# Kernel tuning notes

Hardware: AMD Instinct MI355X
Metric: run time of the kernel (lower is better)

Reference implementation:

```python
import jax, jax.numpy as jnp
import numpy as np

GRID_SIZE = 5
SPLINE_ORDER = 3
IN_FEAT = 320   # 32 * 10
OUT_FEAT = 2048 # 32 * 64
BN_EPS = 1e-3


def make_grid():
    # efficient-kan grid buffer: (in_features, grid_size + 2*spline_order + 1)
    h = 2.0 / GRID_SIZE  # grid_range = [-1, 1]
    g = jnp.arange(-SPLINE_ORDER, GRID_SIZE + SPLINE_ORDER + 1, dtype=jnp.float32) * h - 1.0
    return jnp.broadcast_to(g, (IN_FEAT, g.shape[0]))  # (320, 12)


def b_splines(x, grid):
    # x: (B, In) -> bases: (B, In, grid_size + spline_order)
    x = x[..., None]  # (B, In, 1)
    bases = ((x >= grid[:, :-1]) & (x < grid[:, 1:])).astype(x.dtype)
    for k in range(1, SPLINE_ORDER + 1):
        left = (x - grid[:, : -(k + 1)]) / (grid[:, k:-1] - grid[:, : -(k + 1)])
        right = (grid[:, k + 1:] - x) / (grid[:, k + 1:] - grid[:, 1:-k])
        bases = left * bases[..., :-1] + right * bases[..., 1:]
    return bases


def setup_inputs() -> dict:
    key = jax.random.key(0)
    ks = jax.random.split(key, 8)
    N = 40000
    inputs = jax.random.normal(ks[0], (N, 32, 10), dtype=jnp.float32)
    linear_w = jax.random.normal(ks[1], (64, 10), dtype=jnp.float32) * 0.1
    base_weight = jax.random.normal(ks[2], (OUT_FEAT, IN_FEAT), dtype=jnp.float32) * 0.02
    spline_weight = jax.random.normal(ks[3], (OUT_FEAT, IN_FEAT, GRID_SIZE + SPLINE_ORDER), dtype=jnp.float32) * 0.02
    spline_scaler = jax.random.normal(ks[4], (OUT_FEAT, IN_FEAT), dtype=jnp.float32) * 0.1 + 1.0
    bn_gamma = jax.random.normal(ks[5], (64,), dtype=jnp.float32) * 0.1 + 1.0
    bn_beta = jax.random.normal(ks[6], (64,), dtype=jnp.float32) * 0.1
    bn_mean = jnp.zeros((64,), dtype=jnp.float32)
    bn_var = jax.random.uniform(ks[7], (64,), dtype=jnp.float32, minval=0.5, maxval=1.5)
    return {
        "inputs": inputs,
        "linear_w": linear_w,
        "base_weight": base_weight,
        "spline_weight": spline_weight,
        "spline_scaler": spline_scaler,
        "bn_gamma": bn_gamma,
        "bn_beta": bn_beta,
        "bn_mean": bn_mean,
        "bn_var": bn_var,
    }


def reference(inputs, linear_w, base_weight, spline_weight, spline_scaler,
              bn_gamma, bn_beta, bn_mean, bn_var):
    N = inputs.shape[0]
    # plain linear path: (N, 32, 10) -> (N, 32, 64). (The torch chunking over
    # self.part is mathematically identical to one matmul.)
    x_linear = jnp.einsum('npi,oi->npo', inputs, linear_w)
    # KAN path on flattened pillars: (N, 320)
    xk = inputs.reshape(N, IN_FEAT)
    grid = make_grid()
    base_out = jnp.matmul(jax.nn.silu(xk), base_weight.T)  # (N, 2048)
    bases = b_splines(xk, grid)  # (N, 320, 8)
    scaled_spline_w = (spline_weight * spline_scaler[..., None]).reshape(OUT_FEAT, -1)
    spline_out = jnp.matmul(bases.reshape(N, -1), scaled_spline_w.T)  # (N, 2048)
    x_kan = (base_out + spline_out).reshape(N, 32, 64)
    x = x_linear + x_kan
    # BatchNorm1d over the channel (last) dim, inference mode, eps=1e-3
    inv_std = jax.lax.rsqrt(bn_var + BN_EPS)
    x = (x - bn_mean) * (inv_std * bn_gamma) + bn_beta
    x = jax.nn.relu(x)
    x_max = jnp.max(x, axis=1, keepdims=True)  # (N, 1, 64)
    x_rep = jnp.broadcast_to(x_max, x.shape)   # repeat over 32 points
    return jnp.concatenate([x, x_rep], axis=2)  # (N, 32, 128)
```

## Files before the change

kernel.cpp:

```cpp
#include <hip/hip_runtime.h>
#include <cstdint>
#include <math.h>

#define IN_FEAT 320
#define OUT_FEAT 2048
#define NB 8
#define KSIL 320
#define KTOT 2880
#define BM 128
#define BN 128
#define BK 32
#define LDA 40
#define BN_EPS 1e-3f
#define A_OFF ((size_t)16 << 20)

typedef __bf16 bf16;
typedef __attribute__((ext_vector_type(8))) __bf16 bf16x8;
typedef __attribute__((ext_vector_type(4))) float f32x4;

__device__ __forceinline__ void bspline8(float xv, float* b) {
    float xc = (xv + 2.2f) * 2.5f;
    float cf = floorf(xc);
    int c = (int)cf;
    float t = xc - cf;
    float omt = 1.0f - t;
    float t2 = t * t, t3 = t2 * t;
    float w0 = omt * omt * omt * (1.0f / 6.0f);
    float w1 = (3.0f * t3 - 6.0f * t2 + 4.0f) * (1.0f / 6.0f);
    float w2 = (-3.0f * t3 + 3.0f * t2 + 3.0f * t + 1.0f) * (1.0f / 6.0f);
    float w3 = t3 * (1.0f / 6.0f);
    if (xc < 0.0f) { w0 = w1 = w2 = w3 = 0.0f; }
#pragma unroll
    for (int j = 0; j < 8; ++j) {
        int d = c - j;
        b[j] = (d == 3) ? w0 : (d == 2) ? w1 : (d == 1) ? w2 : (d == 0) ? w3 : 0.0f;
    }
}

__device__ __forceinline__ bf16x8 pack8(const float* f) {
    bf16x8 v;
#pragma unroll
    for (int j = 0; j < 8; ++j) v[j] = (bf16)f[j];
    return v;
}

__device__ __forceinline__ void gl2lds16(const bf16* g, bf16* l) {
    __builtin_amdgcn_global_load_lds(
        (const __attribute__((address_space(1))) void*)g,
        (__attribute__((address_space(3))) void*)l, 16, 0, 0);
}

__global__ __launch_bounds__(256) void prep_w(const float* __restrict__ bw,
                                              const float* __restrict__ sw,
                                              const float* __restrict__ ss,
                                              bf16* __restrict__ W) {
    const int k = blockIdx.x * 256 + threadIdx.x;
    const int o = blockIdx.y;
    if (k >= KTOT) return;
    float w;
    if (k < KSIL) {
        w = bw[o * IN_FEAT + k];
    } else {
        const int s = k - KSIL;
        const int i = s >> 3, j = s & 7;
        w = sw[(o * IN_FEAT + i) * NB + j] * ss[o * IN_FEAT + i];
    }
    W[o * KTOT + k] = (bf16)w;
}

__global__ __launch_bounds__(256) void prep_a(const float* __restrict__ x,
                                              bf16* __restrict__ A, int total) {
    const int t = blockIdx.x * 256 + threadIdx.x;
    if (t >= total) return;
    const int row = t / IN_FEAT;
    const int f = t - row * IN_FEAT;
    const float xv = x[t];
    A[(size_t)row * KTOT + f] = (bf16)(xv / (1.0f + __expf(-xv)));
    float b[8];
    bspline8(xv, b);
    *(bf16x8*)&A[(size_t)row * KTOT + KSIL + f * 8] = pack8(b);
}

__global__ __launch_bounds__(256)
void pfn_gemm_ws(const float* __restrict__ x, const bf16* __restrict__ A,
                 const bf16* __restrict__ W, const float* __restrict__ lw,
                 const float* __restrict__ gamma, const float* __restrict__ beta,
                 const float* __restrict__ mean, const float* __restrict__ var,
                 float* __restrict__ out, int N, int nbx) {
    __shared__ bf16 As[BM * BK];
    __shared__ bf16 Bs[BN * BK];

    const int blk = blockIdx.x;
    const int sid = blk >> 9;
    const int t = blk & 511;
    const int by = t >> 5;
    const int bx = (sid << 5) + (t & 31);
    if (bx >= nbx) return;

    const int row0 = bx * BM;
    const int col0 = by * BN;
    const int tid = threadIdx.x;
    const int wave = tid >> 6;
    const int lane = tid & 63;
    const int wr = wave >> 1;
    const int wc = wave & 1;
    const int l15 = lane & 15;
    const int quad = lane >> 4;

    const int r0 = tid >> 2;
    const int s0 = tid & 3;
    const int g0 = s0 ^ ((r0 >> 1) & 3);
    const bf16* a0 = A + (size_t)(row0 + r0) * KTOT + g0 * 8;
    const bf16* a1 = a0 + (size_t)64 * KTOT;
    const bf16* b0 = W + (size_t)(col0 + r0) * KTOT + g0 * 8;
    const bf16* b1 = b0 + (size_t)64 * KTOT;
    bf16* lA0 = As + tid * 8;
    bf16* lA1 = As + (tid + 256) * 8;
    bf16* lB0 = Bs + tid * 8;
    bf16* lB1 = Bs + (tid + 256) * 8;

    const int sfr = quad ^ ((l15 >> 1) & 3);

    f32x4 acc[4][4] = {};

    for (int kc = 0; kc < KTOT; kc += BK) {
        __syncthreads();
        gl2lds16(a0 + kc, lA0);
        gl2lds16(a1 + kc, lA1);
        gl2lds16(b0 + kc, lB0);
        gl2lds16(b1 + kc, lB1);
        __syncthreads();
        bf16x8 af[4], bv[4];
#pragma unroll
        for (int i = 0; i < 4; ++i)
            af[i] = *(const bf16x8*)&As[(wr * 64 + i * 16 + l15) * BK + sfr * 8];
#pragma unroll
        for (int j = 0; j < 4; ++j)
            bv[j] = *(const bf16x8*)&Bs[(wc * 64 + j * 16 + l15) * BK + sfr * 8];
#pragma unroll
        for (int i = 0; i < 4; ++i)
#pragma unroll
            for (int j = 0; j < 4; ++j)
                acc[i][j] = __builtin_amdgcn_mfma_f32_16x16x32_bf16(af[i], bv[j],
                                                                   acc[i][j], 0, 0, 0);
    }

    const int p = by * 2 + wc;
    float sc[4], sh[4];
#pragma unroll
    for (int j = 0; j < 4; ++j) {
        const int c = j * 16 + l15;
        const float s = rsqrtf(var[c] + BN_EPS) * gamma[c];
        sc[j] = s;
        sh[j] = beta[c] - mean[c] * s;
    }
#pragma unroll
    for (int i = 0; i < 4; ++i) {
#pragma unroll
        for (int reg = 0; reg < 4; ++reg) {
            const int row = row0 + wr * 64 + i * 16 + quad * 4 + reg;
            if (row >= N) continue;
            float xq[10];
            const float* xp = &x[(size_t)row * IN_FEAT + p * 10];
#pragma unroll
            for (int q = 0; q < 10; ++q) xq[q] = xp[q];
#pragma unroll
            for (int j = 0; j < 4; ++j) {
                const int c = j * 16 + l15;
                float v = acc[i][j][reg];
#pragma unroll
                for (int q = 0; q < 10; ++q) v = fmaf(xq[q], lw[c * 10 + q], v);
                v = fmaxf(v * sc[j] + sh[j], 0.0f);
                out[((size_t)row * 32 + p) * 128 + c] = v;
            }
        }
    }
}

template <bool HASW>
__global__ __launch_bounds__(256)
void pfn_gemm(const float* __restrict__ x, const bf16* __restrict__ W,
              const float* __restrict__ bw, const float* __restrict__ sw,
              const float* __restrict__ ss, const float* __restrict__ lw,
              const float* __restrict__ gamma, const float* __restrict__ beta,
              const float* __restrict__ mean, const float* __restrict__ var,
              float* __restrict__ out, int N) {
    __shared__ bf16 As[BM * LDA];
    __shared__ bf16 Bs[BN * LDA];
    const int tid = threadIdx.x;
    const int row0 = blockIdx.x * BM;
    const int col0 = blockIdx.y * BN;
    const int wave = tid >> 6;
    const int lane = tid & 63;
    const int wr = wave >> 1;
    const int wc = wave & 1;
    const int l15 = lane & 15;
    const int quad = lane >> 4;
    f32x4 acc[4][4] = {};
    auto stage_b = [&](int kc) {
        const int ol = tid >> 1;
        const int k0 = (tid & 1) * 16;
        if (HASW) {
            const bf16x8* src = (const bf16x8*)&W[(size_t)(col0 + ol) * KTOT + kc + k0];
            *(bf16x8*)&Bs[ol * LDA + k0] = src[0];
            *(bf16x8*)&Bs[ol * LDA + k0 + 8] = src[1];
        } else {
            const int o = col0 + ol;
#pragma unroll
            for (int u = 0; u < 16; ++u) {
                const int gk = kc + k0 + u;
                float w;
                if (gk < KSIL) {
                    w = bw[o * IN_FEAT + gk];
                } else {
                    const int s = gk - KSIL;
                    const int i = s >> 3, j = s & 7;
                    w = sw[(o * IN_FEAT + i) * NB + j] * ss[o * IN_FEAT + i];
                }
                Bs[ol * LDA + k0 + u] = (bf16)w;
            }
        }
    };
    auto mma_step = [&]() {
        bf16x8 af[4], bv[4];
#pragma unroll
        for (int i = 0; i < 4; ++i)
            af[i] = *(const bf16x8*)&As[(wr * 64 + i * 16 + l15) * LDA + quad * 8];
#pragma unroll
        for (int j = 0; j < 4; ++j)
            bv[j] = *(const bf16x8*)&Bs[(wc * 64 + j * 16 + l15) * LDA + quad * 8];
#pragma unroll
        for (int i = 0; i < 4; ++i)
#pragma unroll
            for (int j = 0; j < 4; ++j)
                acc[i][j] = __builtin_amdgcn_mfma_f32_16x16x32_bf16(af[i], bv[j],
                                                                   acc[i][j], 0, 0, 0);
    };
    for (int kc = 0; kc < KSIL; kc += BK) {
        __syncthreads();
        stage_b(kc);
        {
            const int r = tid >> 1;
            const int k0 = (tid & 1) * 16;
            const int row = row0 + r;
            float v[16];
            if (row < N) {
                const float* xp = &x[(size_t)row * IN_FEAT + kc + k0];
#pragma unroll
                for (int u = 0; u < 16; ++u) {
                    const float xv = xp[u];
                    v[u] = xv / (1.0f + __expf(-xv));
                }
            } else {
#pragma unroll
                for (int u = 0; u < 16; ++u) v[u] = 0.0f;
            }
            *(bf16x8*)&As[r * LDA + k0] = pack8(v);
            *(bf16x8*)&As[r * LDA + k0 + 8] = pack8(v + 8);
        }
        __syncthreads();
        mma_step();
    }
    for (int kc = KSIL; kc < KTOT; kc += BK) {
        __syncthreads();
        stage_b(kc);
        {
            const int i0 = (kc - KSIL) >> 3;
#pragma unroll
            for (int s = 0; s < 2; ++s) {
                const int task = tid + s * 256;
                const int r = task >> 2;
                const int f = task & 3;
                const int row = row0 + r;
                float b[8];
                if (row < N) {
                    bspline8(x[(size_t)row * IN_FEAT + i0 + f], b);
                } else {
#pragma unroll
                    for (int j = 0; j < 8; ++j) b[j] = 0.0f;
                }
                *(bf16x8*)&As[r * LDA + f * 8] = pack8(b);
            }
        }
        __syncthreads();
        mma_step();
    }
    const int p = blockIdx.y * 2 + wc;
    float sc[4], sh[4];
#pragma unroll
    for (int j = 0; j < 4; ++j) {
        const int c = j * 16 + l15;
        const float s = rsqrtf(var[c] + BN_EPS) * gamma[c];
        sc[j] = s;
        sh[j] = beta[c] - mean[c] * s;
    }
#pragma unroll
    for (int i = 0; i < 4; ++i) {
#pragma unroll
        for (int reg = 0; reg < 4; ++reg) {
            const int row = row0 + wr * 64 + i * 16 + quad * 4 + reg;
            if (row >= N) continue;
            float xq[10];
            const float* xp = &x[(size_t)row * IN_FEAT + p * 10];
#pragma unroll
            for (int q = 0; q < 10; ++q) xq[q] = xp[q];
#pragma unroll
            for (int j = 0; j < 4; ++j) {
                const int c = j * 16 + l15;
                float v = acc[i][j][reg];
#pragma unroll
                for (int q = 0; q < 10; ++q) v = fmaf(xq[q], lw[c * 10 + q], v);
                v = fmaxf(v * sc[j] + sh[j], 0.0f);
                out[((size_t)row * 32 + p) * 128 + c] = v;
            }
        }
    }
}

__global__ __launch_bounds__(256) void pfn_maxcat(float* __restrict__ out, int N) {
    const int n = blockIdx.x;
    const int c = threadIdx.x & 63;
    const int g = threadIdx.x >> 6;
    __shared__ float red[4][64];
    float m = 0.0f;
    for (int pp = g; pp < 32; pp += 4)
        m = fmaxf(m, out[((size_t)n * 32 + pp) * 128 + c]);
    red[g][c] = m;
    __syncthreads();
    m = fmaxf(fmaxf(red[0][c], red[1][c]), fmaxf(red[2][c], red[3][c]));
    for (int pp = g; pp < 32; pp += 4)
        out[((size_t)n * 32 + pp) * 128 + 64 + c] = m;
}

extern "C" void kernel_launch(void* const* d_in, const int* in_sizes, int n_in,
                              void* d_out, int out_size, void* d_ws, size_t ws_size,
                              hipStream_t stream) {
    const float* x     = (const float*)d_in[0];
    const float* lw    = (const float*)d_in[1];
    const float* bw    = (const float*)d_in[2];
    const float* sw    = (const float*)d_in[3];
    const float* ss    = (const float*)d_in[4];
    const float* gamma = (const float*)d_in[5];
    const float* beta  = (const float*)d_in[6];
    const float* mean  = (const float*)d_in[7];
    const float* var   = (const float*)d_in[8];
    float* out = (float*)d_out;

    const int N = in_sizes[0] / IN_FEAT;
    const int nbx = (N + BM - 1) / BM;
    const size_t w_bytes = (size_t)OUT_FEAT * KTOT * sizeof(bf16);
    const size_t a_bytes = (size_t)nbx * BM * KTOT * sizeof(bf16);

    if (ws_size >= A_OFF + a_bytes) {
        bf16* W = (bf16*)d_ws;
        bf16* A = (bf16*)((char*)d_ws + A_OFF);
        prep_w<<<dim3((KTOT + 255) / 256, OUT_FEAT), 256, 0, stream>>>(bw, sw, ss, W);
        prep_a<<<(N * IN_FEAT + 255) / 256, 256, 0, stream>>>(x, A, N * IN_FEAT);
        const int supers = (nbx + 31) / 32;
        pfn_gemm_ws<<<supers * 512, 256, 0, stream>>>(x, A, W, lw, gamma, beta,
                                                      mean, var, out, N, nbx);
    } else if (ws_size >= w_bytes) {
        bf16* W = (bf16*)d_ws;
        prep_w<<<dim3((KTOT + 255) / 256, OUT_FEAT), 256, 0, stream>>>(bw, sw, ss, W);
        pfn_gemm<true><<<dim3(nbx, OUT_FEAT / BN), 256, 0, stream>>>(
            x, W, bw, sw, ss, lw, gamma, beta, mean, var, out, N);
    } else {
        pfn_gemm<false><<<dim3(nbx, OUT_FEAT / BN), 256, 0, stream>>>(
            x, nullptr, bw, sw, ss, lw, gamma, beta, mean, var, out, N);
    }
    pfn_maxcat<<<N, 256, 0, stream>>>(out, N);
}
```

Before: 1.697 ms.

## Triple-buffer LDS tiles with async global-to-LDS prefetch in GEMM main loop

Replaces the single-buffered K loop, which had two barriers per step and no overlap between loads and MFMA, with a three-stage LDS ring. Tiles two steps ahead are issued via global-to-LDS loads and gated with explicit vmcnt waits, so global latency hides behind matrix math. MFMA sections are also wrapped in s_setprio to favour the compute waves. LDS use triples to 48KB per block, which may lower occupancy.

```diff
diff --git a/kernel.cpp b/kernel.cpp
--- a/kernel.cpp
+++ b/kernel.cpp
@@ -10,6 +10,7 @@
 #define BM 128
 #define BN 128
 #define BK 32
+#define NT (KTOT / BK)
 #define LDA 40
 #define BN_EPS 1e-3f
 #define A_OFF ((size_t)16 << 20)
@@ -17,6 +18,9 @@
 typedef __bf16 bf16;
 typedef __attribute__((ext_vector_type(8))) __bf16 bf16x8;
 typedef __attribute__((ext_vector_type(4))) float f32x4;
+
+#define VMW(n) asm volatile("s_waitcnt vmcnt(" #n ")" ::: "memory")
+#define BAR() __builtin_amdgcn_s_barrier()
 
 __device__ __forceinline__ void bspline8(float xv, float* b) {
     float xc = (xv + 2.2f) * 2.5f;
@@ -87,14 +91,14 @@
                  const float* __restrict__ gamma, const float* __restrict__ beta,
                  const float* __restrict__ mean, const float* __restrict__ var,
                  float* __restrict__ out, int N, int nbx) {
-    __shared__ bf16 As[BM * BK];
-    __shared__ bf16 Bs[BN * BK];
+    __shared__ bf16 As[3][BM * BK];
+    __shared__ bf16 Bs[3][BN * BK];
 
     const int blk = blockIdx.x;
     const int sid = blk >> 9;
-    const int t = blk & 511;
-    const int by = t >> 5;
-    const int bx = (sid << 5) + (t & 31);
+    const int tt = blk & 511;
+    const int by = tt >> 5;
+    const int bx = (sid << 5) + (tt & 31);
     if (bx >= nbx) return;
 
     const int row0 = bx * BM;
@@ -114,36 +118,55 @@
     const bf16* a1 = a0 + (size_t)64 * KTOT;
     const bf16* b0 = W + (size_t)(col0 + r0) * KTOT + g0 * 8;
     const bf16* b1 = b0 + (size_t)64 * KTOT;
-    bf16* lA0 = As + tid * 8;
-    bf16* lA1 = As + (tid + 256) * 8;
-    bf16* lB0 = Bs + tid * 8;
-    bf16* lB1 = Bs + (tid + 256) * 8;
 
     const int sfr = quad ^ ((l15 >> 1) & 3);
 
     f32x4 acc[4][4] = {};
 
-    for (int kc = 0; kc < KTOT; kc += BK) {
-        __syncthreads();
-        gl2lds16(a0 + kc, lA0);
-        gl2lds16(a1 + kc, lA1);
-        gl2lds16(b0 + kc, lB0);
-        gl2lds16(b1 + kc, lB1);
-        __syncthreads();
+    auto stage = [&](int b, int kc) {
+        gl2lds16(a0 + kc, &As[b][tid * 8]);
+        gl2lds16(a1 + kc, &As[b][(tid + 256) * 8]);
+        gl2lds16(b0 + kc, &Bs[b][tid * 8]);
+        gl2lds16(b1 + kc, &Bs[b][(tid + 256) * 8]);
+    };
+    auto step = [&](int b) {
         bf16x8 af[4], bv[4];
 #pragma unroll
         for (int i = 0; i < 4; ++i)
-            af[i] = *(const bf16x8*)&As[(wr * 64 + i * 16 + l15) * BK + sfr * 8];
+            af[i] = *(const bf16x8*)&As[b][(wr * 64 + i * 16 + l15) * BK + sfr * 8];
 #pragma unroll
         for (int j = 0; j < 4; ++j)
-            bv[j] = *(const bf16x8*)&Bs[(wc * 64 + j * 16 + l15) * BK + sfr * 8];
+            bv[j] = *(const bf16x8*)&Bs[b][(wc * 64 + j * 16 + l15) * BK + sfr * 8];
+        __builtin_amdgcn_s_setprio(1);
 #pragma unroll
         for (int i = 0; i < 4; ++i)
 #pragma unroll
             for (int j = 0; j < 4; ++j)
                 acc[i][j] = __builtin_amdgcn_mfma_f32_16x16x32_bf16(af[i], bv[j],
                                                                    acc[i][j], 0, 0, 0);
-    }
+        __builtin_amdgcn_s_setprio(0);
+    };
+
+    stage(0, 0);
+    stage(1, BK);
+
+    int kc = 0;
+#pragma unroll 1
+    for (int u = 0; u < NT / 3 - 1; ++u) {
+        stage(2, kc + 2 * BK); VMW(8); BAR();
+        step(0); BAR();
+        stage(0, kc + 3 * BK); VMW(8); BAR();
+        step(1); BAR();
+        stage(1, kc + 4 * BK); VMW(8); BAR();
+        step(2); BAR();
+        kc += 3 * BK;
+    }
+    stage(2, kc + 2 * BK); VMW(8); BAR();
+    step(0); BAR();
+    VMW(4); BAR();
+    step(1); BAR();
+    VMW(0); BAR();
+    step(2);
 
     const int p = by * 2 + wc;
     float sc[4], sh[4];
```

After: 1.712 ms. Within noise of the previous version (+0.8%).
